# Kernel optimization log

Hardware: AMD Instinct MI355X
Metric: run time of the kernel (lower is better)

Reference implementation:

```python
import jax, jax.numpy as jnp
import numpy as np

NUM_EMBEDDINGS = 512
EMBEDDING_DIM = 64
BETA = 0.25


def setup_inputs() -> dict:
    key = jax.random.key(0)
    k1, k2 = jax.random.split(key)
    latent_z = jax.random.normal(k1, (32, EMBEDDING_DIM, 64, 64), dtype=jnp.float32)
    # nn.Embedding init: uniform(-1/K, 1/K)
    scale = 1.0 / NUM_EMBEDDINGS
    embedding = jax.random.uniform(k2, (NUM_EMBEDDINGS, EMBEDDING_DIM), dtype=jnp.float32,
                                   minval=-scale, maxval=scale)
    return {"latent_z": latent_z, "embedding": embedding}


def reference(latent_z, embedding):
    # [B, C, H, W] -> [B, H, W, C]
    z = jnp.transpose(latent_z, (0, 2, 3, 1))
    B, H, W, D = z.shape
    flat_z = z.reshape(-1, D)  # [N, D]

    # squared L2 distances via expansion: ||z||^2 + ||e||^2 - 2 z.e
    dist = (jnp.sum(flat_z ** 2, axis=1, keepdims=True)
            + jnp.sum(embedding ** 2, axis=1)
            - 2.0 * flat_z @ embedding.T)  # [N, K]

    idx = jnp.argmin(dist, axis=1)  # [N]
    encodings = jax.nn.one_hot(idx, NUM_EMBEDDINGS, dtype=flat_z.dtype)  # [N, K]

    # gather codes (same math as one_hot @ embedding)
    quantized = embedding[idx].reshape(B, H, W, D)

    quant_loss = (jnp.mean((jax.lax.stop_gradient(quantized) - z) ** 2)
                  + BETA * jnp.mean((quantized - jax.lax.stop_gradient(z)) ** 2))

    # straight-through estimator
    quantized_st = z + jax.lax.stop_gradient(quantized - z)

    mean_enc = jnp.mean(encodings, axis=0)
    perplexity = jnp.exp(-jnp.sum(mean_enc * jnp.log(mean_enc + 1e-10)))

    quantized_out = jnp.transpose(quantized_st, (0, 3, 1, 2))  # back to [B, C, H, W]
    return quant_loss, quantized_out, perplexity, encodings, idx[:, None]
```

## Files before the change

### kernel.cpp

```cpp
#include <hip/hip_runtime.h>
#include <math.h>

#define NPIX   131072
#define KCODES 512
#define DIM    64
#define HW     4096
#define CHW    262144

#define O_Q    1ll
#define O_PERP 8388609ll
#define O_ENC  8388610ll
#define O_IDX  75497474ll


__device__ __forceinline__ float np_sumsq64(const float (&x)[64]) {
#pragma clang fp contract(off)
  float r0 = x[0]*x[0], r1 = x[1]*x[1], r2 = x[2]*x[2], r3 = x[3]*x[3];
  float r4 = x[4]*x[4], r5 = x[5]*x[5], r6 = x[6]*x[6], r7 = x[7]*x[7];
#pragma unroll
  for (int i = 8; i < 64; i += 8) {
    r0 += x[i+0]*x[i+0];
    r1 += x[i+1]*x[i+1];
    r2 += x[i+2]*x[i+2];
    r3 += x[i+3]*x[i+3];
    r4 += x[i+4]*x[i+4];
    r5 += x[i+5]*x[i+5];
    r6 += x[i+6]*x[i+6];
    r7 += x[i+7]*x[i+7];
  }
  return ((r0+r1)+(r2+r3))+((r4+r5)+(r6+r7));
}

__global__ void vq_prep(const float* __restrict__ emb, float* __restrict__ ws) {
  const int t = threadIdx.x;
  if (t == 0) ws[0] = 0.0f;
  ((unsigned*)ws)[1 + t] = 0u;
  float x[64];
  const float* e = emb + t * DIM;
#pragma unroll
  for (int d = 0; d < 64; ++d) x[d] = e[d];
  ws[513 + t] = np_sumsq64(x);
}

__global__ __launch_bounds__(256)
__attribute__((amdgpu_waves_per_eu(2, 2)))
void vq_main(
    const float* __restrict__ z, const float* __restrict__ emb,
    float* __restrict__ out, float* __restrict__ ws)
{
  __shared__ float ET_s[16 * 512];
  __shared__ float z_l[64 * 64];
  __shared__ float esq_l[512];
  __shared__ float zsq_l[64];
  __shared__ int   ridx_l[64];

  const int t   = threadIdx.x;
  const int ci  = t & 31;
  const int pi  = t >> 5;
  const int blk = blockIdx.x;
  const int n0  = blk * 64;
  const int b   = n0 >> 12;
  const int hw0 = n0 & 4095;
  const float* zg = z + (size_t)b * CHW + hw0;

  esq_l[t]       = ws[513 + t];
  esq_l[t + 256] = ws[513 + 256 + t];

  {
    const int i     = t & 15;
    const int dbase = t >> 4;
#pragma unroll
    for (int r = 0; r < 4; ++r) {
      const int d = dbase + 16 * r;
      const float4 v = *(const float4*)(zg + (size_t)d * HW + 4 * i);
      *(float4*)&z_l[d * 64 + 4 * i] = v;
    }
  }
  __syncthreads();

  if (t < 64) {
    float x[64];
#pragma unroll
    for (int d = 0; d < 64; ++d) x[d] = z_l[d * 64 + t];
    zsq_l[t] = np_sumsq64(x);
  }

  float acc[8][16];
#pragma unroll
  for (int j = 0; j < 8; ++j)
#pragma unroll
    for (int c = 0; c < 16; ++c) acc[j][c] = 0.0f;

  for (int s = 0; s < 4; ++s) {
    __syncthreads();
#pragma unroll
    for (int h = 0; h < 2; ++h) {
      const int c = t + 256 * h;
      const float* er = emb + (size_t)c * 64 + 16 * s;
      const float4 v0 = *(const float4*)(er + 0);
      const float4 v1 = *(const float4*)(er + 4);
      const float4 v2 = *(const float4*)(er + 8);
      const float4 v3 = *(const float4*)(er + 12);
      float tmp[16] = {v0.x, v0.y, v0.z, v0.w, v1.x, v1.y, v1.z, v1.w,
                       v2.x, v2.y, v2.z, v2.w, v3.x, v3.y, v3.z, v3.w};
#pragma unroll
      for (int dl = 0; dl < 16; ++dl) ET_s[dl * 512 + c] = tmp[dl];
    }
    __syncthreads();

#pragma unroll 2
    for (int dl = 0; dl < 16; ++dl) {
      const float* zp = &z_l[(16 * s + dl) * 64 + 8 * pi];
      const float4 za0 = *(const float4*)(zp + 0);
      const float4 za1 = *(const float4*)(zp + 4);
      const float* ep = &ET_s[dl * 512 + 4 * ci];
      const float4 e0 = *(const float4*)(ep + 0);
      const float4 e1 = *(const float4*)(ep + 128);
      const float4 e2 = *(const float4*)(ep + 256);
      const float4 e3 = *(const float4*)(ep + 384);
      const float zr[8]  = {za0.x, za0.y, za0.z, za0.w, za1.x, za1.y, za1.z, za1.w};
      const float er_[16] = {e0.x, e0.y, e0.z, e0.w, e1.x, e1.y, e1.z, e1.w,
                             e2.x, e2.y, e2.z, e2.w, e3.x, e3.y, e3.z, e3.w};
#pragma unroll
      for (int j = 0; j < 8; ++j)
#pragma unroll
        for (int c = 0; c < 16; ++c)
          acc[j][c] = fmaf(zr[j], er_[c], acc[j][c]);
    }
  }

  float bd[8];
  int   bk[8];
#pragma unroll
  for (int j = 0; j < 8; ++j) { bd[j] = INFINITY; bk[j] = 0; }
#pragma unroll
  for (int q = 0; q < 4; ++q)
#pragma unroll
    for (int r = 0; r < 4; ++r) {
      const int k = 128 * q + 4 * ci + r;
      const float eq = esq_l[k];
#pragma unroll
      for (int j = 0; j < 8; ++j) {
        const float dist = (zsq_l[8 * pi + j] + eq) - 2.0f * acc[j][4 * q + r];
        if (dist < bd[j]) { bd[j] = dist; bk[j] = k; }
      }
    }
#pragma unroll
  for (int m = 16; m >= 1; m >>= 1) {
#pragma unroll
    for (int j = 0; j < 8; ++j) {
      const float od = __shfl_xor(bd[j], m, 64);
      const int   ok = __shfl_xor(bk[j], m, 64);
      if (od < bd[j] || (od == bd[j] && ok < bk[j])) { bd[j] = od; bk[j] = ok; }
    }
  }
  if (ci == 0) {
#pragma unroll
    for (int j = 0; j < 8; ++j) ridx_l[8 * pi + j] = bk[j];
  }
  __syncthreads();

  if (t < 64) {
    const int n = n0 + t;
    const int k = ridx_l[t];
    out[O_IDX + n] = (float)k;
    const float* e0 = emb + ((size_t)k << 6);
    float* q0 = out + O_Q + (size_t)b * CHW + hw0 + t;
    float lsum = 0.0f;
#pragma unroll
    for (int d = 0; d < 64; ++d) {
      const float ev = e0[d];
      const float df = ev - z_l[d * 64 + t];
      lsum = fmaf(df, df, lsum);
      q0[(size_t)d * HW] = ev;
    }
#pragma unroll
    for (int off = 32; off > 0; off >>= 1) lsum += __shfl_down(lsum, off, 64);
    if (t == 0) atomicAdd(ws, lsum);
    atomicAdd((unsigned*)ws + 1 + k, 1u);
  }

  float2* enc = (float2*)(out + O_ENC) + (size_t)n0 * 256;
  for (int i = t; i < 64 * 256; i += 256) {
    const int r  = i >> 8;
    const int c2 = i & 255;
    const int bv = ridx_l[r];
    float2 v = make_float2(0.0f, 0.0f);
    if ((bv >> 1) == c2) {
      if (bv & 1) v.y = 1.0f; else v.x = 1.0f;
    }
    enc[i] = v;
  }
}

__global__ void vq_fin(float* __restrict__ out, const float* __restrict__ ws) {
  __shared__ float red[8];
  const int t = threadIdx.x;
  const unsigned* counts = (const unsigned*)ws + 1;
  const float p = (float)counts[t] * (1.0f / 131072.0f);
  float h = p * logf(p + 1e-10f);
#pragma unroll
  for (int off = 32; off > 0; off >>= 1) h += __shfl_down(h, off, 64);
  if ((t & 63) == 0) red[t >> 6] = h;
  __syncthreads();
  if (t == 0) {
    float H = 0.0f;
#pragma unroll
    for (int w = 0; w < 8; ++w) H += red[w];
    out[O_PERP] = expf(-H);
    out[0] = 1.25f * ws[0] * (1.0f / 8388608.0f);
  }
}

extern "C" void kernel_launch(void* const* d_in, const int* in_sizes, int n_in,
                              void* d_out, int out_size, void* d_ws, size_t ws_size,
                              hipStream_t stream) {
  const float* z   = (const float*)d_in[0];
  const float* emb = (const float*)d_in[1];
  float* out = (float*)d_out;
  float* ws  = (float*)d_ws;

  vq_prep<<<1, 512, 0, stream>>>(emb, ws);
  vq_main<<<2048, 256, 0, stream>>>(z, emb, out, ws);
  vq_fin<<<1, 512, 0, stream>>>(out, ws);
}
```

Baseline: 452.5 us.

## Split codebook distance pass into two halves to cut registers and raise occupancy

The distance GEMM now runs in two passes over 256-code halves, with an 8x8 accumulator per thread instead of 8x16. This halves accumulator registers and the shared embedding tile, and the waves-per-EU hint goes from 2 to 4. The quantized-output write and loss sum are also spread over all four waves instead of one, with a shared-memory reduction before a single atomic. The cost is twice as many embedding staging rounds and barriers per block.

New measurement: 452.1 us. No clear change (-0.1%).

```diff
diff --git a/kernel.cpp b/kernel.cpp
--- a/kernel.cpp
+++ b/kernel.cpp
@@ -43,16 +43,17 @@
 }
 
 __global__ __launch_bounds__(256)
-__attribute__((amdgpu_waves_per_eu(2, 2)))
+__attribute__((amdgpu_waves_per_eu(4, 4)))
 void vq_main(
     const float* __restrict__ z, const float* __restrict__ emb,
     float* __restrict__ out, float* __restrict__ ws)
 {
-  __shared__ float ET_s[16 * 512];
+  __shared__ float ET_s[16 * 256];
   __shared__ float z_l[64 * 64];
   __shared__ float esq_l[512];
   __shared__ float zsq_l[64];
   __shared__ int   ridx_l[64];
+  __shared__ float wsum[4];
 
   const int t   = threadIdx.x;
   const int ci  = t & 31;
@@ -64,7 +65,7 @@
   const float* zg = z + (size_t)b * CHW + hw0;
 
   esq_l[t]       = ws[513 + t];
-  esq_l[t + 256] = ws[513 + 256 + t];
+  esq_l[t + 256] = ws[769 + t];
 
   {
     const int i     = t & 15;
@@ -85,66 +86,67 @@
     zsq_l[t] = np_sumsq64(x);
   }
 
-  float acc[8][16];
-#pragma unroll
-  for (int j = 0; j < 8; ++j)
-#pragma unroll
-    for (int c = 0; c < 16; ++c) acc[j][c] = 0.0f;
-
-  for (int s = 0; s < 4; ++s) {
-    __syncthreads();
-#pragma unroll
-    for (int h = 0; h < 2; ++h) {
-      const int c = t + 256 * h;
-      const float* er = emb + (size_t)c * 64 + 16 * s;
-      const float4 v0 = *(const float4*)(er + 0);
-      const float4 v1 = *(const float4*)(er + 4);
-      const float4 v2 = *(const float4*)(er + 8);
-      const float4 v3 = *(const float4*)(er + 12);
-      float tmp[16] = {v0.x, v0.y, v0.z, v0.w, v1.x, v1.y, v1.z, v1.w,
-                       v2.x, v2.y, v2.z, v2.w, v3.x, v3.y, v3.z, v3.w};
-#pragma unroll
-      for (int dl = 0; dl < 16; ++dl) ET_s[dl * 512 + c] = tmp[dl];
-    }
-    __syncthreads();
-
-#pragma unroll 2
-    for (int dl = 0; dl < 16; ++dl) {
-      const float* zp = &z_l[(16 * s + dl) * 64 + 8 * pi];
-      const float4 za0 = *(const float4*)(zp + 0);
-      const float4 za1 = *(const float4*)(zp + 4);
-      const float* ep = &ET_s[dl * 512 + 4 * ci];
-      const float4 e0 = *(const float4*)(ep + 0);
-      const float4 e1 = *(const float4*)(ep + 128);
-      const float4 e2 = *(const float4*)(ep + 256);
-      const float4 e3 = *(const float4*)(ep + 384);
-      const float zr[8]  = {za0.x, za0.y, za0.z, za0.w, za1.x, za1.y, za1.z, za1.w};
-      const float er_[16] = {e0.x, e0.y, e0.z, e0.w, e1.x, e1.y, e1.z, e1.w,
-                             e2.x, e2.y, e2.z, e2.w, e3.x, e3.y, e3.z, e3.w};
-#pragma unroll
-      for (int j = 0; j < 8; ++j)
-#pragma unroll
-        for (int c = 0; c < 16; ++c)
-          acc[j][c] = fmaf(zr[j], er_[c], acc[j][c]);
-    }
-  }
-
   float bd[8];
   int   bk[8];
 #pragma unroll
   for (int j = 0; j < 8; ++j) { bd[j] = INFINITY; bk[j] = 0; }
-#pragma unroll
-  for (int q = 0; q < 4; ++q)
-#pragma unroll
-    for (int r = 0; r < 4; ++r) {
-      const int k = 128 * q + 4 * ci + r;
-      const float eq = esq_l[k];
-#pragma unroll
-      for (int j = 0; j < 8; ++j) {
-        const float dist = (zsq_l[8 * pi + j] + eq) - 2.0f * acc[j][4 * q + r];
-        if (dist < bd[j]) { bd[j] = dist; bk[j] = k; }
+
+  for (int H = 0; H < 2; ++H) {
+    float acc[8][8];
+#pragma unroll
+    for (int j = 0; j < 8; ++j)
+#pragma unroll
+      for (int c = 0; c < 8; ++c) acc[j][c] = 0.0f;
+
+    for (int s = 0; s < 4; ++s) {
+      __syncthreads();
+      {
+        const float* er = emb + (size_t)(256 * H + t) * 64 + 16 * s;
+        const float4 v0 = *(const float4*)(er + 0);
+        const float4 v1 = *(const float4*)(er + 4);
+        const float4 v2 = *(const float4*)(er + 8);
+        const float4 v3 = *(const float4*)(er + 12);
+        float tmp[16] = {v0.x, v0.y, v0.z, v0.w, v1.x, v1.y, v1.z, v1.w,
+                         v2.x, v2.y, v2.z, v2.w, v3.x, v3.y, v3.z, v3.w};
+#pragma unroll
+        for (int dl = 0; dl < 16; ++dl) ET_s[dl * 256 + t] = tmp[dl];
       }
-    }
+      __syncthreads();
+
+#pragma unroll 2
+      for (int dl = 0; dl < 16; ++dl) {
+        const float* zp = &z_l[(16 * s + dl) * 64 + 8 * pi];
+        const float4 za0 = *(const float4*)(zp + 0);
+        const float4 za1 = *(const float4*)(zp + 4);
+        const float* ep = &ET_s[dl * 256 + 4 * ci];
+        const float4 e0 = *(const float4*)(ep + 0);
+        const float4 e1 = *(const float4*)(ep + 128);
+        const float zr[8] = {za0.x, za0.y, za0.z, za0.w,
+                             za1.x, za1.y, za1.z, za1.w};
+        const float er_[8] = {e0.x, e0.y, e0.z, e0.w,
+                              e1.x, e1.y, e1.z, e1.w};
+#pragma unroll
+        for (int j = 0; j < 8; ++j)
+#pragma unroll
+          for (int c = 0; c < 8; ++c)
+            acc[j][c] = fmaf(zr[j], er_[c], acc[j][c]);
+      }
+    }
+
+#pragma unroll
+    for (int q = 0; q < 2; ++q)
+#pragma unroll
+      for (int r = 0; r < 4; ++r) {
+        const int k = 256 * H + 128 * q + 4 * ci + r;
+        const float eq = esq_l[k];
+#pragma unroll
+        for (int j = 0; j < 8; ++j) {
+          const float dist = (zsq_l[8 * pi + j] + eq) - 2.0f * acc[j][4 * q + r];
+          if (dist < bd[j]) { bd[j] = dist; bk[j] = k; }
+        }
+      }
+  }
+
 #pragma unroll
   for (int m = 16; m >= 1; m >>= 1) {
 #pragma unroll
@@ -161,24 +163,32 @@
   __syncthreads();
 
   if (t < 64) {
-    const int n = n0 + t;
     const int k = ridx_l[t];
-    out[O_IDX + n] = (float)k;
+    out[O_IDX + n0 + t] = (float)k;
+    atomicAdd((unsigned*)ws + 1 + k, 1u);
+  }
+
+  {
+    const int px = t & 63;
+    const int dq = t >> 6;
+    const int k  = ridx_l[px];
     const float* e0 = emb + ((size_t)k << 6);
-    float* q0 = out + O_Q + (size_t)b * CHW + hw0 + t;
+    float* q0 = out + O_Q + (size_t)b * CHW + hw0 + px;
     float lsum = 0.0f;
 #pragma unroll
-    for (int d = 0; d < 64; ++d) {
+    for (int j = 0; j < 16; ++j) {
+      const int d = dq * 16 + j;
       const float ev = e0[d];
-      const float df = ev - z_l[d * 64 + t];
+      const float df = ev - z_l[d * 64 + px];
       lsum = fmaf(df, df, lsum);
       q0[(size_t)d * HW] = ev;
     }
 #pragma unroll
     for (int off = 32; off > 0; off >>= 1) lsum += __shfl_down(lsum, off, 64);
-    if (t == 0) atomicAdd(ws, lsum);
-    atomicAdd((unsigned*)ws + 1 + k, 1u);
-  }
+    if ((t & 63) == 0) wsum[t >> 6] = lsum;
+  }
+  __syncthreads();
+  if (t == 0) atomicAdd(ws, (wsum[0] + wsum[1]) + (wsum[2] + wsum[3]));
 
   float2* enc = (float2*)(out + O_ENC) + (size_t)n0 * 256;
   for (int i = t; i < 64 * 256; i += 256) {
```

## Halve pixels per block and re-tile distance GEMM for higher occupancy

Applied to the files above, without the earlier changes.

Each block now handles 32 pixels instead of 64, using a 16-pixel by 4-code register tile per thread. Z values are read straight from global memory rather than staged in LDS, and waves_per_eu goes from 2 to 4 with twice as many blocks. The argmin reduction becomes a full-wave shuffle plus a cross-wave LDS merge, and the loss and quantized write are spread across all threads. The aim is more latency hiding and less register pressure, at the cost of reloading the codebook into LDS twice as often and repeating global z loads across the 128 threads of each half-block.

Measured after the change: 578.3 us. 1.28x slower.

```diff
diff --git a/kernel.cpp b/kernel.cpp
--- a/kernel.cpp
+++ b/kernel.cpp
@@ -43,56 +43,47 @@
 }
 
 __global__ __launch_bounds__(256)
-__attribute__((amdgpu_waves_per_eu(2, 2)))
+__attribute__((amdgpu_waves_per_eu(4, 4)))
 void vq_main(
     const float* __restrict__ z, const float* __restrict__ emb,
     float* __restrict__ out, float* __restrict__ ws)
 {
   __shared__ float ET_s[16 * 512];
-  __shared__ float z_l[64 * 64];
   __shared__ float esq_l[512];
-  __shared__ float zsq_l[64];
-  __shared__ int   ridx_l[64];
+  __shared__ float zsq_l[32];
+  __shared__ int   ridx_l[32];
+  __shared__ float md[4][16];
+  __shared__ int   mk[4][16];
+  __shared__ float wsum[4];
 
   const int t   = threadIdx.x;
-  const int ci  = t & 31;
-  const int pi  = t >> 5;
+  const int u   = t & 127;
+  const int g   = t >> 7;
   const int blk = blockIdx.x;
-  const int n0  = blk * 64;
+  const int n0  = blk * 32;
   const int b   = n0 >> 12;
   const int hw0 = n0 & 4095;
-  const float* zg = z + (size_t)b * CHW + hw0;
+  const float* zblk = z + (size_t)b * CHW + hw0;
+  const float* zgb  = zblk + 16 * g;
 
   esq_l[t]       = ws[513 + t];
-  esq_l[t + 256] = ws[513 + 256 + t];
-
-  {
-    const int i     = t & 15;
-    const int dbase = t >> 4;
-#pragma unroll
-    for (int r = 0; r < 4; ++r) {
-      const int d = dbase + 16 * r;
-      const float4 v = *(const float4*)(zg + (size_t)d * HW + 4 * i);
-      *(float4*)&z_l[d * 64 + 4 * i] = v;
-    }
-  }
-  __syncthreads();
-
-  if (t < 64) {
+  esq_l[t + 256] = ws[769 + t];
+
+  if (t < 32) {
     float x[64];
 #pragma unroll
-    for (int d = 0; d < 64; ++d) x[d] = z_l[d * 64 + t];
+    for (int d = 0; d < 64; ++d) x[d] = zblk[(size_t)d * HW + t];
     zsq_l[t] = np_sumsq64(x);
   }
 
-  float acc[8][16];
-#pragma unroll
-  for (int j = 0; j < 8; ++j)
-#pragma unroll
-    for (int c = 0; c < 16; ++c) acc[j][c] = 0.0f;
+  float acc[16][4];
+#pragma unroll
+  for (int j = 0; j < 16; ++j)
+#pragma unroll
+    for (int r = 0; r < 4; ++r) acc[j][r] = 0.0f;
 
   for (int s = 0; s < 4; ++s) {
-    __syncthreads();
+    if (s) __syncthreads();
 #pragma unroll
     for (int h = 0; h < 2; ++h) {
       const int c = t + 256 * h;
@@ -110,78 +101,91 @@
 
 #pragma unroll 2
     for (int dl = 0; dl < 16; ++dl) {
-      const float* zp = &z_l[(16 * s + dl) * 64 + 8 * pi];
-      const float4 za0 = *(const float4*)(zp + 0);
-      const float4 za1 = *(const float4*)(zp + 4);
-      const float* ep = &ET_s[dl * 512 + 4 * ci];
-      const float4 e0 = *(const float4*)(ep + 0);
-      const float4 e1 = *(const float4*)(ep + 128);
-      const float4 e2 = *(const float4*)(ep + 256);
-      const float4 e3 = *(const float4*)(ep + 384);
-      const float zr[8]  = {za0.x, za0.y, za0.z, za0.w, za1.x, za1.y, za1.z, za1.w};
-      const float er_[16] = {e0.x, e0.y, e0.z, e0.w, e1.x, e1.y, e1.z, e1.w,
-                             e2.x, e2.y, e2.z, e2.w, e3.x, e3.y, e3.z, e3.w};
-#pragma unroll
-      for (int j = 0; j < 8; ++j)
-#pragma unroll
-        for (int c = 0; c < 16; ++c)
-          acc[j][c] = fmaf(zr[j], er_[c], acc[j][c]);
-    }
-  }
-
-  float bd[8];
-  int   bk[8];
-#pragma unroll
-  for (int j = 0; j < 8; ++j) { bd[j] = INFINITY; bk[j] = 0; }
-#pragma unroll
-  for (int q = 0; q < 4; ++q)
+      const int d = 16 * s + dl;
+      const float* zr = zgb + (size_t)d * HW;
+      const float4 z0 = *(const float4*)(zr + 0);
+      const float4 z1 = *(const float4*)(zr + 4);
+      const float4 z2 = *(const float4*)(zr + 8);
+      const float4 z3 = *(const float4*)(zr + 12);
+      const float4 e4 = *(const float4*)&ET_s[dl * 512 + 4 * u];
+      const float zv[16] = {z0.x, z0.y, z0.z, z0.w, z1.x, z1.y, z1.z, z1.w,
+                            z2.x, z2.y, z2.z, z2.w, z3.x, z3.y, z3.z, z3.w};
+      const float ev[4] = {e4.x, e4.y, e4.z, e4.w};
+#pragma unroll
+      for (int j = 0; j < 16; ++j)
+#pragma unroll
+        for (int r = 0; r < 4; ++r)
+          acc[j][r] = fmaf(zv[j], ev[r], acc[j][r]);
+    }
+  }
+
+  float bd[16];
+  int   bk[16];
+#pragma unroll
+  for (int j = 0; j < 16; ++j) {
+    const float zq = zsq_l[16 * g + j];
+    float best = INFINITY; int bi = 0;
 #pragma unroll
     for (int r = 0; r < 4; ++r) {
-      const int k = 128 * q + 4 * ci + r;
-      const float eq = esq_l[k];
-#pragma unroll
-      for (int j = 0; j < 8; ++j) {
-        const float dist = (zsq_l[8 * pi + j] + eq) - 2.0f * acc[j][4 * q + r];
-        if (dist < bd[j]) { bd[j] = dist; bk[j] = k; }
-      }
-    }
-#pragma unroll
-  for (int m = 16; m >= 1; m >>= 1) {
-#pragma unroll
-    for (int j = 0; j < 8; ++j) {
+      const int k = 4 * u + r;
+      const float dist = (zq + esq_l[k]) - 2.0f * acc[j][r];
+      if (dist < best) { best = dist; bi = k; }
+    }
+    bd[j] = best; bk[j] = bi;
+  }
+#pragma unroll
+  for (int m = 32; m >= 1; m >>= 1) {
+#pragma unroll
+    for (int j = 0; j < 16; ++j) {
       const float od = __shfl_xor(bd[j], m, 64);
       const int   ok = __shfl_xor(bk[j], m, 64);
       if (od < bd[j] || (od == bd[j] && ok < bk[j])) { bd[j] = od; bk[j] = ok; }
     }
   }
-  if (ci == 0) {
-#pragma unroll
-    for (int j = 0; j < 8; ++j) ridx_l[8 * pi + j] = bk[j];
-  }
-  __syncthreads();
-
-  if (t < 64) {
-    const int n = n0 + t;
-    const int k = ridx_l[t];
-    out[O_IDX + n] = (float)k;
-    const float* e0 = emb + ((size_t)k << 6);
-    float* q0 = out + O_Q + (size_t)b * CHW + hw0 + t;
+  {
+    const int w = t >> 6;
+    if ((t & 63) == 0) {
+#pragma unroll
+      for (int j = 0; j < 16; ++j) { md[w][j] = bd[j]; mk[w][j] = bk[j]; }
+    }
+  }
+  __syncthreads();
+  if (t < 32) {
+    const int g2 = t >> 4, pl = t & 15;
+    const float d0 = md[2 * g2][pl];     const int k0 = mk[2 * g2][pl];
+    const float d1 = md[2 * g2 + 1][pl]; const int k1 = mk[2 * g2 + 1][pl];
+    const int kb = (d1 < d0) ? k1 : k0;
+    ridx_l[t] = kb;
+    out[O_IDX + n0 + t] = (float)kb;
+    atomicAdd((unsigned*)ws + 1 + kb, 1u);
+  }
+  __syncthreads();
+
+  {
+    const int px = t & 31;
+    const int dq = t >> 5;
+    const int kq = ridx_l[px];
+    const float* e0 = emb + ((size_t)kq << 6) + 8 * dq;
+    float* q0 = out + O_Q + (size_t)b * CHW + hw0 + px;
+    const float* zq = zblk + px;
     float lsum = 0.0f;
 #pragma unroll
-    for (int d = 0; d < 64; ++d) {
-      const float ev = e0[d];
-      const float df = ev - z_l[d * 64 + t];
+    for (int j = 0; j < 8; ++j) {
+      const int d = 8 * dq + j;
+      const float ev = e0[j];
+      const float df = ev - zq[(size_t)d * HW];
       lsum = fmaf(df, df, lsum);
       q0[(size_t)d * HW] = ev;
     }
 #pragma unroll
     for (int off = 32; off > 0; off >>= 1) lsum += __shfl_down(lsum, off, 64);
-    if (t == 0) atomicAdd(ws, lsum);
-    atomicAdd((unsigned*)ws + 1 + k, 1u);
-  }
+    if ((t & 63) == 0) wsum[t >> 6] = lsum;
+  }
+  __syncthreads();
+  if (t == 0) atomicAdd(ws, (wsum[0] + wsum[1]) + (wsum[2] + wsum[3]));
 
   float2* enc = (float2*)(out + O_ENC) + (size_t)n0 * 256;
-  for (int i = t; i < 64 * 256; i += 256) {
+  for (int i = t; i < 32 * 256; i += 256) {
     const int r  = i >> 8;
     const int c2 = i & 255;
     const int bv = ridx_l[r];
@@ -221,6 +225,6 @@
   float* ws  = (float*)d_ws;
 
   vq_prep<<<1, 512, 0, stream>>>(emb, ws);
-  vq_main<<<2048, 256, 0, stream>>>(z, emb, out, ws);
+  vq_main<<<4096, 256, 0, stream>>>(z, emb, out, ws);
   vq_fin<<<1, 512, 0, stream>>>(out, ws);
 }
```
